# Optimization experiments

Hardware: AMD Instinct MI355X
Metric: run time of the kernel (lower is better)

The kernel has to match this reference:

```python
import jax, jax.numpy as jnp
import numpy as np

DIM = 1024
DIM_HEAD = 128
HEADS = 8
DIM_INNER = DIM_HEAD * HEADS


def setup_inputs() -> dict:
    key = jax.random.key(0)
    k_x, k_qkv, k_out = jax.random.split(key, 3)
    x = jax.random.normal(k_x, (2, 2048, DIM), dtype=jnp.float32)
    gamma = jnp.ones((DIM,), dtype=jnp.float32)
    # nn.Linear weights stored as [out, in]; init ~ U(-1/sqrt(in), 1/sqrt(in))
    w_qkv = jax.random.uniform(k_qkv, (DIM_INNER * 3, DIM), dtype=jnp.float32,
                               minval=-1.0, maxval=1.0) / np.sqrt(DIM)
    w_out = jax.random.uniform(k_out, (DIM, DIM_INNER), dtype=jnp.float32,
                               minval=-1.0, maxval=1.0) / np.sqrt(DIM_INNER)
    return {"x": x, "gamma": gamma, "w_qkv": w_qkv, "w_out": w_out}


def reference(x, gamma, w_qkv, w_out):
    scale_norm = DIM ** 0.5
    scale_attn = DIM_HEAD ** -0.5
    # RMSNorm as written: F.normalize (L2) * sqrt(dim) * gamma
    l2 = jnp.sqrt(jnp.sum(x * x, axis=-1, keepdims=True))
    xn = x / jnp.maximum(l2, 1e-12) * scale_norm * gamma
    # QKV projection: [b, n, 3*h*d]
    qkv = jnp.einsum('bnc,fc->bnf', xn, w_qkv)
    b, n, _ = qkv.shape
    qkv = qkv.reshape(b, n, 3, HEADS, DIM_HEAD)
    q, k, v = (qkv[:, :, 0], qkv[:, :, 1], qkv[:, :, 2])  # [b, n, h, d]
    q = q * scale_attn
    sim = jnp.einsum('bihd,bjhd->bhij', q, k)
    causal_mask = jnp.triu(jnp.ones((n, n), dtype=bool), k=1)
    neg = -jnp.finfo(sim.dtype).max
    sim = jnp.where(causal_mask, neg, sim)
    attn = jax.nn.softmax(sim, axis=-1)
    out = jnp.einsum('bhij,bjhd->bihd', attn, v)
    out = out.reshape(b, n, DIM_INNER)  # merge heads: b n (h d)
    return jnp.einsum('bnf,cf->bnc', out, w_out)
```

## Files before the change

### kernel.cpp

```cpp
#include <hip/hip_runtime.h>

#define SEQ 2048
#define NTOK 4096
#define DIM 1024
#define FQKV 3072
#define SC_ATTN 0.08838834764831843f
#define SC_Q (0.08838834764831843f * 1.4426950408889634f)
#define SC_NORM 32.0f

typedef short short8 __attribute__((ext_vector_type(8)));
typedef float f32x4 __attribute__((ext_vector_type(4)));
typedef unsigned short u16x4 __attribute__((ext_vector_type(4)));

__device__ __forceinline__ unsigned short f2bf(float f) {
    unsigned int u = __float_as_uint(f);
    u += 0x7fffu + ((u >> 16) & 1u);
    return (unsigned short)(u >> 16);
}
__device__ __forceinline__ void gl_lds16(const void* g, void* l) {
    __builtin_amdgcn_global_load_lds((const __attribute__((address_space(1))) void*)g,
                                     (__attribute__((address_space(3))) void*)l, 16, 0, 0);
}

__global__ __launch_bounds__(256) void l2norm_bf16(const float* __restrict__ x,
                                                   const float* __restrict__ gamma,
                                                   unsigned short* __restrict__ xn) {
    int token = blockIdx.x;
    float4 v = ((const float4*)(x + (size_t)token * DIM))[threadIdx.x];
    float ss = v.x * v.x + v.y * v.y + v.z * v.z + v.w * v.w;
#pragma unroll
    for (int off = 32; off > 0; off >>= 1) ss += __shfl_down(ss, off);
    __shared__ float wsum[4];
    if ((threadIdx.x & 63) == 0) wsum[threadIdx.x >> 6] = ss;
    __syncthreads();
    float tot = wsum[0] + wsum[1] + wsum[2] + wsum[3];
    float sc = SC_NORM / fmaxf(sqrtf(tot), 1e-12f);
    float4 g = ((const float4*)gamma)[threadIdx.x];
    u16x4 o;
    o.x = f2bf(v.x * sc * g.x);
    o.y = f2bf(v.y * sc * g.y);
    o.z = f2bf(v.z * sc * g.z);
    o.w = f2bf(v.w * sc * g.w);
    ((u16x4*)(xn + (size_t)token * DIM))[threadIdx.x] = o;
}

__global__ __launch_bounds__(256) void wconv2(const float* __restrict__ wa, unsigned short* __restrict__ oa, int na4,
                                              const float* __restrict__ wb, unsigned short* __restrict__ ob, int nb4) {
    int i = blockIdx.x * 256 + threadIdx.x;
    const float* w; unsigned short* o; int idx;
    if (i < na4) { w = wa; o = oa; idx = i; }
    else { idx = i - na4; if (idx >= nb4) return; w = wb; o = ob; }
    float4 v = ((const float4*)w)[idx];
    u16x4 r;
    r.x = f2bf(v.x); r.y = f2bf(v.y); r.z = f2bf(v.z); r.w = f2bf(v.w);
    ((u16x4*)o)[idx] = r;
}

template<int C_MODE, int TM>
__global__ __launch_bounds__(256) void gemm_bf16(const unsigned short* __restrict__ A,
                                                 const unsigned short* __restrict__ B,
                                                 void* __restrict__ Cv,
                                                 int M, int N, int K) {
    constexpr int MF = TM / 32;
    __shared__ unsigned short As[TM * 64];
    __shared__ unsigned short Bs[128 * 64];

    int lin = blockIdx.y * gridDim.x + blockIdx.x;
    int nwg = gridDim.x * gridDim.y;
    int w = (lin & 7) * (nwg >> 3) + (lin >> 3);
    int bx = w % gridDim.x, by = w / gridDim.x;

    const int bn = bx * 128, bm = by * TM;
    const int tid = threadIdx.x, lane = tid & 63, wv = tid >> 6;
    const int wr = wv >> 1, wc = wv & 1;
    const int l15 = lane & 15, g = lane >> 4;

    f32x4 acc[MF][4] = {};

    auto stage = [&](int k0) {
#pragma unroll
        for (int ia = 0; ia < TM / 32; ++ia) {
            int ci = ia * 256 + wv * 64 + lane;
            int row = ci >> 3, cc = ci & 7;
            int co = (cc ^ (row & 7)) << 3;
            gl_lds16(A + (size_t)(bm + row) * K + k0 + co, &As[(ia * 256 + wv * 64) * 8]);
        }
#pragma unroll
        for (int ib = 0; ib < 4; ++ib) {
            int ci = ib * 256 + wv * 64 + lane;
            int row = ci >> 3, cc = ci & 7;
            int co = (cc ^ (row & 7)) << 3;
            gl_lds16(B + (size_t)(bn + row) * K + k0 + co, &Bs[(ib * 256 + wv * 64) * 8]);
        }
    };

    stage(0);
    asm volatile("s_waitcnt vmcnt(0)\ns_barrier" ::: "memory");

    for (int k0 = 0; k0 < K; k0 += 64) {
        short8 af[2][MF], bf[2][4];
#pragma unroll
        for (int ks = 0; ks < 2; ++ks) {
#pragma unroll
            for (int f = 0; f < MF; ++f) {
                int ra = wr * (TM / 2) + f * 16 + l15;
                af[ks][f] = *(const short8*)&As[ra * 64 + (((ks * 4 + g) ^ (ra & 7)) << 3)];
            }
#pragma unroll
            for (int f = 0; f < 4; ++f) {
                int rb = wc * 64 + f * 16 + l15;
                bf[ks][f] = *(const short8*)&Bs[rb * 64 + (((ks * 4 + g) ^ (rb & 7)) << 3)];
            }
        }
        asm volatile("s_waitcnt lgkmcnt(0)\ns_barrier" ::: "memory");
        if (k0 + 64 < K) stage(k0 + 64);
#pragma unroll
        for (int ks = 0; ks < 2; ++ks)
#pragma unroll
            for (int i = 0; i < MF; ++i)
#pragma unroll
                for (int j = 0; j < 4; ++j)
                    acc[i][j] = __builtin_amdgcn_mfma_f32_16x16x32_bf16(af[ks][i], bf[ks][j], acc[i][j], 0, 0, 0);
        asm volatile("s_waitcnt vmcnt(0)\ns_barrier" ::: "memory");
    }

    if (C_MODE == 0) {
        float* C = (float*)Cv;
#pragma unroll
        for (int i = 0; i < MF; ++i)
#pragma unroll
            for (int j = 0; j < 4; ++j)
#pragma unroll
                for (int v = 0; v < 4; ++v) {
                    int row = bm + wr * (TM / 2) + i * 16 + g * 4 + v;
                    int col = bn + wc * 64 + j * 16 + l15;
                    C[(size_t)row * N + col] = acc[i][j][v];
                }
    } else {
        unsigned short* C = (unsigned short*)Cv;
        float s = (bn < 1024) ? SC_Q : 1.0f;
#pragma unroll
        for (int i = 0; i < MF; ++i)
#pragma unroll
            for (int j = 0; j < 4; ++j)
#pragma unroll
                for (int v = 0; v < 4; ++v) {
                    int row = bm + wr * (TM / 2) + i * 16 + g * 4 + v;
                    int col = bn + wc * 64 + j * 16 + l15;
                    C[(size_t)row * N + col] = f2bf(acc[i][j][v] * s);
                }
    }
}

__global__ __launch_bounds__(256) void transpose_v(const unsigned short* __restrict__ qkv,
                                                   unsigned short* __restrict__ vt) {
    __shared__ unsigned short T[64][72];
    const int t0 = blockIdx.x * 64, d0 = blockIdx.y * 64, bh = blockIdx.z;
    const int b = bh >> 3, h = bh & 7;
    const int tid = threadIdx.x;
#pragma unroll
    for (int p = 0; p < 2; ++p) {
        int r = p * 32 + (tid >> 3), c = tid & 7;
        *(short8*)&T[r][c * 8] =
            *(const short8*)(qkv + (size_t)(b * SEQ + t0 + r) * FQKV + 2048 + h * 128 + d0 + c * 8);
    }
    __syncthreads();
#pragma unroll
    for (int p = 0; p < 2; ++p) {
        int d = p * 32 + (tid >> 3), c = tid & 7;
        short8 v;
#pragma unroll
        for (int j = 0; j < 8; ++j) v[j] = (short)T[c * 8 + j][d];
        *(short8*)(vt + (size_t)(bh * 128 + d0 + d) * SEQ + t0 + c * 8) = v;
    }
}

__global__ __launch_bounds__(256) void attn_mfma(const unsigned short* __restrict__ qkv,
                                                 const unsigned short* __restrict__ vt,
                                                 unsigned short* __restrict__ ao,
                                                 float* __restrict__ po,
                                                 float* __restrict__ pml) {
    __shared__ unsigned short Ks[64 * 128];
    __shared__ unsigned short Vs[128 * 64];
    __shared__ unsigned short Ps[4][16 * 64];
    const int h = blockIdx.y, b = blockIdx.z;
    const int x = blockIdx.x;
    int qblk, jb0, jb1, split, slot;
    if (x < 32) {
        qblk = 31 - (x >> 1);
        int s = x & 1;
        int T = qblk + 1, half = (T + 1) >> 1;
        jb0 = s ? half : 0;
        jb1 = s ? T : half;
        split = 1;
        slot = ((b * 8 + h) * 16 + (qblk - 16)) * 2 + s;
    } else {
        qblk = 47 - x;
        jb0 = 0; jb1 = qblk + 1;
        split = 0; slot = 0;
    }
    const int tid = threadIdx.x, lane = tid & 63, wv = tid >> 6;
    const int l15 = lane & 15, g = lane >> 4;
    const int q0 = qblk * 64;
    const int qrow = q0 + wv * 16 + l15;

    auto stageK = [&](int jb) {
#pragma unroll
        for (int inst = 0; inst < 4; ++inst) {
            int ci = inst * 256 + wv * 64 + lane;
            int rowk = ci >> 4, ck = ci & 15;
            gl_lds16(qkv + (size_t)(b * SEQ + jb * 64 + rowk) * FQKV + 1024 + h * 128
                         + ((ck ^ (rowk & 7)) << 3),
                     &Ks[(inst * 256 + wv * 64) * 8]);
        }
    };
    auto stageV = [&](int jb) {
#pragma unroll
        for (int inst = 0; inst < 4; ++inst) {
            int ci = inst * 256 + wv * 64 + lane;
            int rowv = ci >> 3, cv = ci & 7;
            gl_lds16(vt + (size_t)((b * 8 + h) * 128 + rowv) * SEQ + jb * 64
                        + ((cv ^ (rowv & 7)) << 3),
                     &Vs[(inst * 256 + wv * 64) * 8]);
        }
    };

    short8 qf[4];
    {
        const unsigned short* qb = qkv + (size_t)(b * SEQ + qrow) * FQKV + h * 128;
#pragma unroll
        for (int ks = 0; ks < 4; ++ks) qf[ks] = *(const short8*)(qb + ks * 32 + g * 8);
    }

    float m_r = -1e30f, l_r = 0.f;
    f32x4 o[8] = {};

    stageK(jb0);
    __syncthreads();

    for (int jb = jb0; jb < jb1; ++jb) {
        stageV(jb);

        f32x4 s[4] = {};
        __builtin_amdgcn_s_setprio(1);
#pragma unroll
        for (int ks = 0; ks < 4; ++ks) {
#pragma unroll
            for (int fi = 0; fi < 4; ++fi) {
                int rk = fi * 16 + l15;
                short8 kf = *(const short8*)&Ks[rk * 128 + (((ks * 4 + g) ^ (rk & 7)) << 3)];
                s[fi] = __builtin_amdgcn_mfma_f32_16x16x32_bf16(kf, qf[ks], s[fi], 0, 0, 0);
            }
        }
        __builtin_amdgcn_s_setprio(0);

        if (jb == qblk) {
#pragma unroll
            for (int fi = 0; fi < 4; ++fi)
#pragma unroll
                for (int v = 0; v < 4; ++v) {
                    int kv = q0 + fi * 16 + g * 4 + v;
                    if (kv > qrow) s[fi][v] = -1e30f;
                }
        }

        float mx = -1e30f;
#pragma unroll
        for (int fi = 0; fi < 4; ++fi)
            mx = fmaxf(mx, fmaxf(fmaxf(s[fi][0], s[fi][1]), fmaxf(s[fi][2], s[fi][3])));
        mx = fmaxf(mx, __shfl_xor(mx, 16));
        mx = fmaxf(mx, __shfl_xor(mx, 32));
        if (__any(mx - m_r > 16.0f)) {
            float Mn = fmaxf(m_r, mx);
            float alpha = exp2f(m_r - Mn);
            l_r *= alpha;
            float av[4];
#pragma unroll
            for (int v = 0; v < 4; ++v) av[v] = __shfl(alpha, g * 4 + v);
#pragma unroll
            for (int fn = 0; fn < 8; ++fn) {
                o[fn][0] *= av[0]; o[fn][1] *= av[1]; o[fn][2] *= av[2]; o[fn][3] *= av[3];
            }
            m_r = Mn;
        }

        float ps = 0.f;
#pragma unroll
        for (int fi = 0; fi < 4; ++fi) {
#pragma unroll
            for (int p2 = 0; p2 < 2; ++p2) {
                float e0 = exp2f(s[fi][2 * p2] - m_r);
                float e1 = exp2f(s[fi][2 * p2 + 1] - m_r);
                ps += e0 + e1;
                unsigned short b0 = f2bf(e0), b1 = f2bf(e1);
                int kv = fi * 16 + g * 4 + 2 * p2;
                int addr = l15 * 64 + (((kv >> 3) ^ (l15 & 7)) << 3) + (kv & 7);
                *(unsigned int*)&Ps[wv][addr] = (unsigned int)b0 | ((unsigned int)b1 << 16);
            }
        }
        ps += __shfl_xor(ps, 16);
        ps += __shfl_xor(ps, 32);
        l_r += ps;

        __syncthreads();
        if (jb + 1 < jb1) stageK(jb + 1);

        __builtin_amdgcn_s_setprio(1);
#pragma unroll
        for (int ks = 0; ks < 2; ++ks) {
            short8 pa = *(const short8*)&Ps[wv][l15 * 64 + (((ks * 4 + g) ^ (l15 & 7)) << 3)];
#pragma unroll
            for (int fn = 0; fn < 8; ++fn) {
                int rv = fn * 16 + l15;
                short8 vf = *(const short8*)&Vs[rv * 64 + (((ks * 4 + g) ^ (rv & 7)) << 3)];
                o[fn] = __builtin_amdgcn_mfma_f32_16x16x32_bf16(pa, vf, o[fn], 0, 0, 0);
            }
        }
        __builtin_amdgcn_s_setprio(0);

        __syncthreads();
    }

    if (split) {
        float* od = po + (size_t)slot * (64 * 128);
#pragma unroll
        for (int fn = 0; fn < 8; ++fn)
#pragma unroll
            for (int v = 0; v < 4; ++v)
                od[(wv * 16 + g * 4 + v) * 128 + fn * 16 + l15] = o[fn][v];
        if (g == 0) {
            pml[(size_t)slot * 128 + wv * 16 + l15] = m_r;
            pml[(size_t)slot * 128 + 64 + wv * 16 + l15] = l_r;
        }
    } else {
        float lv[4];
#pragma unroll
        for (int v = 0; v < 4; ++v) lv[v] = 1.0f / __shfl(l_r, g * 4 + v);
#pragma unroll
        for (int fn = 0; fn < 8; ++fn)
#pragma unroll
            for (int v = 0; v < 4; ++v) {
                int row = b * SEQ + q0 + wv * 16 + g * 4 + v;
                ao[(size_t)row * DIM + h * 128 + fn * 16 + l15] = f2bf(o[fn][v] * lv[v]);
            }
    }
}

__global__ __launch_bounds__(256) void attn_combine(const float* __restrict__ po,
                                                    const float* __restrict__ pml,
                                                    unsigned short* __restrict__ ao) {
    int t = blockIdx.x;
    int qi = t & 15, h = (t >> 4) & 7, b = t >> 7;
    int qblk = 16 + qi;
    int slot0 = ((b * 8 + h) * 16 + qi) * 2;
    int row = threadIdx.x >> 2;
    int dp = threadIdx.x & 3;
    float m0 = pml[(size_t)slot0 * 128 + row];
    float l0 = pml[(size_t)slot0 * 128 + 64 + row];
    float m1 = pml[(size_t)(slot0 + 1) * 128 + row];
    float l1 = pml[(size_t)(slot0 + 1) * 128 + 64 + row];
    float M = fmaxf(m0, m1);
    float w0 = exp2f(m0 - M), w1 = exp2f(m1 - M);
    float inv = 1.0f / (w0 * l0 + w1 * l1);
    w0 *= inv; w1 *= inv;
    const float4* O0 = (const float4*)(po + (size_t)slot0 * 8192 + row * 128 + dp * 32);
    const float4* O1 = (const float4*)(po + (size_t)(slot0 + 1) * 8192 + row * 128 + dp * 32);
    unsigned short* dst = ao + ((size_t)(b * SEQ + qblk * 64 + row)) * DIM + h * 128 + dp * 32;
#pragma unroll
    for (int j = 0; j < 8; ++j) {
        float4 a = O0[j], c = O1[j];
        u16x4 r;
        r.x = f2bf(w0 * a.x + w1 * c.x);
        r.y = f2bf(w0 * a.y + w1 * c.y);
        r.z = f2bf(w0 * a.z + w1 * c.z);
        r.w = f2bf(w0 * a.w + w1 * c.w);
        *(u16x4*)(dst + j * 4) = r;
    }
}

extern "C" void kernel_launch(void* const* d_in, const int* in_sizes, int n_in,
                              void* d_out, int out_size, void* d_ws, size_t ws_size,
                              hipStream_t stream) {
    const float* x     = (const float*)d_in[0];
    const float* gamma = (const float*)d_in[1];
    const float* w_qkv = (const float*)d_in[2];
    const float* w_out = (const float*)d_in[3];

    char* ws = (char*)d_ws;
    unsigned short* qkvb = (unsigned short*)ws;
    unsigned short* vtb  = (unsigned short*)(ws + 25165824);
    unsigned short* xnb  = (unsigned short*)(ws + 33554432);
    unsigned short* wqb  = (unsigned short*)(ws + 41943040);
    unsigned short* wob  = (unsigned short*)(ws + 48234496);
    unsigned short* aob  = (unsigned short*)(ws + 50331648);
    float*          pml  = (float*)(ws + 58720256);
    float*          po   = (float*)d_out;

    wconv2<<<4096, 256, 0, stream>>>(w_qkv, wqb, 786432, w_out, wob, 262144);
    l2norm_bf16<<<4096, 256, 0, stream>>>(x, gamma, xnb);
    gemm_bf16<1, 128><<<dim3(24, 32), 256, 0, stream>>>(xnb, wqb, qkvb, NTOK, FQKV, DIM);
    transpose_v<<<dim3(32, 2, 16), 256, 0, stream>>>(qkvb, vtb);
    attn_mfma<<<dim3(48, 8, 2), 256, 0, stream>>>(qkvb, vtb, aob, po, pml);
    attn_combine<<<256, 256, 0, stream>>>(po, pml, aob);
    gemm_bf16<0, 64><<<dim3(8, 64), 256, 0, stream>>>(aob, wob, (float*)d_out, NTOK, DIM, DIM);
}
```

Measured before the change: 119.9 us.

## Rebalance causal attention with variable-width KV splits and bf16 partials

Attention work is now split more finely: query blocks 28-31 get 4 KV splits, blocks 18-27 get 3, blocks 9-17 get 2, and the rest run unsplit, with 73 blocks per head instead of 48. The goal is to even out the triangular causal workload across CUs and cut tail time. Partial outputs are stored as bf16 instead of fp32 to halve scratch traffic. The combine kernel is generalised to merge 2-4 partials. The weight conversion and the L2 norm now run in one prep launch. Costs are more combine work and extra rounding of the partials to bf16.

```diff
diff --git a/kernel.cpp b/kernel.cpp
--- a/kernel.cpp
+++ b/kernel.cpp
@@ -4,7 +4,6 @@
 #define NTOK 4096
 #define DIM 1024
 #define FQKV 3072
-#define SC_ATTN 0.08838834764831843f
 #define SC_Q (0.08838834764831843f * 1.4426950408889634f)
 #define SC_NORM 32.0f
 
@@ -17,43 +16,49 @@
     u += 0x7fffu + ((u >> 16) & 1u);
     return (unsigned short)(u >> 16);
 }
+__device__ __forceinline__ float bf2f(unsigned short b) {
+    return __uint_as_float(((unsigned int)b) << 16);
+}
 __device__ __forceinline__ void gl_lds16(const void* g, void* l) {
     __builtin_amdgcn_global_load_lds((const __attribute__((address_space(1))) void*)g,
                                      (__attribute__((address_space(3))) void*)l, 16, 0, 0);
 }
 
-__global__ __launch_bounds__(256) void l2norm_bf16(const float* __restrict__ x,
-                                                   const float* __restrict__ gamma,
-                                                   unsigned short* __restrict__ xn) {
-    int token = blockIdx.x;
-    float4 v = ((const float4*)(x + (size_t)token * DIM))[threadIdx.x];
-    float ss = v.x * v.x + v.y * v.y + v.z * v.z + v.w * v.w;
-#pragma unroll
-    for (int off = 32; off > 0; off >>= 1) ss += __shfl_down(ss, off);
-    __shared__ float wsum[4];
-    if ((threadIdx.x & 63) == 0) wsum[threadIdx.x >> 6] = ss;
-    __syncthreads();
-    float tot = wsum[0] + wsum[1] + wsum[2] + wsum[3];
-    float sc = SC_NORM / fmaxf(sqrtf(tot), 1e-12f);
-    float4 g = ((const float4*)gamma)[threadIdx.x];
-    u16x4 o;
-    o.x = f2bf(v.x * sc * g.x);
-    o.y = f2bf(v.y * sc * g.y);
-    o.z = f2bf(v.z * sc * g.z);
-    o.w = f2bf(v.w * sc * g.w);
-    ((u16x4*)(xn + (size_t)token * DIM))[threadIdx.x] = o;
-}
-
-__global__ __launch_bounds__(256) void wconv2(const float* __restrict__ wa, unsigned short* __restrict__ oa, int na4,
-                                              const float* __restrict__ wb, unsigned short* __restrict__ ob, int nb4) {
-    int i = blockIdx.x * 256 + threadIdx.x;
-    const float* w; unsigned short* o; int idx;
-    if (i < na4) { w = wa; o = oa; idx = i; }
-    else { idx = i - na4; if (idx >= nb4) return; w = wb; o = ob; }
-    float4 v = ((const float4*)w)[idx];
-    u16x4 r;
-    r.x = f2bf(v.x); r.y = f2bf(v.y); r.z = f2bf(v.z); r.w = f2bf(v.w);
-    ((u16x4*)o)[idx] = r;
+__global__ __launch_bounds__(256) void prep(const float* __restrict__ x,
+                                            const float* __restrict__ gamma,
+                                            unsigned short* __restrict__ xn,
+                                            const float* __restrict__ wq,
+                                            unsigned short* __restrict__ wqb,
+                                            const float* __restrict__ wo,
+                                            unsigned short* __restrict__ wob) {
+    if (blockIdx.x < 4096) {
+        int token = blockIdx.x;
+        float4 v = ((const float4*)(x + (size_t)token * DIM))[threadIdx.x];
+        float ss = v.x * v.x + v.y * v.y + v.z * v.z + v.w * v.w;
+#pragma unroll
+        for (int off = 32; off > 0; off >>= 1) ss += __shfl_down(ss, off);
+        __shared__ float wsum[4];
+        if ((threadIdx.x & 63) == 0) wsum[threadIdx.x >> 6] = ss;
+        __syncthreads();
+        float tot = wsum[0] + wsum[1] + wsum[2] + wsum[3];
+        float sc = SC_NORM / fmaxf(sqrtf(tot), 1e-12f);
+        float4 g = ((const float4*)gamma)[threadIdx.x];
+        u16x4 o;
+        o.x = f2bf(v.x * sc * g.x);
+        o.y = f2bf(v.y * sc * g.y);
+        o.z = f2bf(v.z * sc * g.z);
+        o.w = f2bf(v.w * sc * g.w);
+        ((u16x4*)(xn + (size_t)token * DIM))[threadIdx.x] = o;
+    } else {
+        int i = (blockIdx.x - 4096) * 256 + threadIdx.x;
+        const float* w; unsigned short* o; int idx;
+        if (i < 786432) { w = wq; o = wqb; idx = i; }
+        else            { w = wo; o = wob; idx = i - 786432; }
+        float4 v = ((const float4*)w)[idx];
+        u16x4 r;
+        r.x = f2bf(v.x); r.y = f2bf(v.y); r.z = f2bf(v.z); r.w = f2bf(v.w);
+        ((u16x4*)o)[idx] = r;
+    }
 }
 
 template<int C_MODE, int TM>
@@ -178,27 +183,23 @@
 __global__ __launch_bounds__(256) void attn_mfma(const unsigned short* __restrict__ qkv,
                                                  const unsigned short* __restrict__ vt,
                                                  unsigned short* __restrict__ ao,
-                                                 float* __restrict__ po,
+                                                 unsigned short* __restrict__ po,
                                                  float* __restrict__ pml) {
     __shared__ unsigned short Ks[64 * 128];
     __shared__ unsigned short Vs[128 * 64];
     __shared__ unsigned short Ps[4][16 * 64];
     const int h = blockIdx.y, b = blockIdx.z;
     const int x = blockIdx.x;
-    int qblk, jb0, jb1, split, slot;
-    if (x < 32) {
-        qblk = 31 - (x >> 1);
-        int s = x & 1;
-        int T = qblk + 1, half = (T + 1) >> 1;
-        jb0 = s ? half : 0;
-        jb1 = s ? T : half;
-        split = 1;
-        slot = ((b * 8 + h) * 16 + (qblk - 16)) * 2 + s;
-    } else {
-        qblk = 47 - x;
-        jb0 = 0; jb1 = qblk + 1;
-        split = 0; slot = 0;
-    }
+    int qblk, s, nsp;
+    if (x < 30)      { qblk = 27 - x / 3;               s = x % 3;  nsp = 3; }
+    else if (x < 46) { int i = x - 30; qblk = 31 - (i >> 2); s = i & 3; nsp = 4; }
+    else if (x < 64) { int i = x - 46; qblk = 17 - (i >> 1); s = i & 1; nsp = 2; }
+    else             { qblk = 72 - x;                   s = 0;      nsp = 1; }
+    const int T = qblk + 1;
+    const int jb0 = (s * T) / nsp, jb1 = ((s + 1) * T) / nsp;
+    const int split = (nsp > 1);
+    const int slot = ((b * 8 + h) << 6) + x;
+
     const int tid = threadIdx.x, lane = tid & 63, wv = tid >> 6;
     const int l15 = lane & 15, g = lane >> 4;
     const int q0 = qblk * 64;
@@ -241,7 +242,7 @@
     for (int jb = jb0; jb < jb1; ++jb) {
         stageV(jb);
 
-        f32x4 s[4] = {};
+        f32x4 sv[4] = {};
         __builtin_amdgcn_s_setprio(1);
 #pragma unroll
         for (int ks = 0; ks < 4; ++ks) {
@@ -249,7 +250,7 @@
             for (int fi = 0; fi < 4; ++fi) {
                 int rk = fi * 16 + l15;
                 short8 kf = *(const short8*)&Ks[rk * 128 + (((ks * 4 + g) ^ (rk & 7)) << 3)];
-                s[fi] = __builtin_amdgcn_mfma_f32_16x16x32_bf16(kf, qf[ks], s[fi], 0, 0, 0);
+                sv[fi] = __builtin_amdgcn_mfma_f32_16x16x32_bf16(kf, qf[ks], sv[fi], 0, 0, 0);
             }
         }
         __builtin_amdgcn_s_setprio(0);
@@ -260,14 +261,14 @@
 #pragma unroll
                 for (int v = 0; v < 4; ++v) {
                     int kv = q0 + fi * 16 + g * 4 + v;
-                    if (kv > qrow) s[fi][v] = -1e30f;
+                    if (kv > qrow) sv[fi][v] = -1e30f;
                 }
         }
 
         float mx = -1e30f;
 #pragma unroll
         for (int fi = 0; fi < 4; ++fi)
-            mx = fmaxf(mx, fmaxf(fmaxf(s[fi][0], s[fi][1]), fmaxf(s[fi][2], s[fi][3])));
+            mx = fmaxf(mx, fmaxf(fmaxf(sv[fi][0], sv[fi][1]), fmaxf(sv[fi][2], sv[fi][3])));
         mx = fmaxf(mx, __shfl_xor(mx, 16));
         mx = fmaxf(mx, __shfl_xor(mx, 32));
         if (__any(mx - m_r > 16.0f)) {
@@ -289,8 +290,8 @@
         for (int fi = 0; fi < 4; ++fi) {
 #pragma unroll
             for (int p2 = 0; p2 < 2; ++p2) {
-                float e0 = exp2f(s[fi][2 * p2] - m_r);
-                float e1 = exp2f(s[fi][2 * p2 + 1] - m_r);
+                float e0 = exp2f(sv[fi][2 * p2] - m_r);
+                float e1 = exp2f(sv[fi][2 * p2 + 1] - m_r);
                 ps += e0 + e1;
                 unsigned short b0 = f2bf(e0), b1 = f2bf(e1);
                 int kv = fi * 16 + g * 4 + 2 * p2;
@@ -322,12 +323,12 @@
     }
 
     if (split) {
-        float* od = po + (size_t)slot * (64 * 128);
+        unsigned short* od = po + (size_t)slot * 8192;
 #pragma unroll
         for (int fn = 0; fn < 8; ++fn)
 #pragma unroll
             for (int v = 0; v < 4; ++v)
-                od[(wv * 16 + g * 4 + v) * 128 + fn * 16 + l15] = o[fn][v];
+                od[(wv * 16 + g * 4 + v) * 128 + fn * 16 + l15] = f2bf(o[fn][v]);
         if (g == 0) {
             pml[(size_t)slot * 128 + wv * 16 + l15] = m_r;
             pml[(size_t)slot * 128 + 64 + wv * 16 + l15] = l_r;
@@ -346,35 +347,50 @@
     }
 }
 
-__global__ __launch_bounds__(256) void attn_combine(const float* __restrict__ po,
+__global__ __launch_bounds__(256) void attn_combine(const unsigned short* __restrict__ po,
                                                     const float* __restrict__ pml,
                                                     unsigned short* __restrict__ ao) {
-    int t = blockIdx.x;
-    int qi = t & 15, h = (t >> 4) & 7, b = t >> 7;
-    int qblk = 16 + qi;
-    int slot0 = ((b * 8 + h) * 16 + qi) * 2;
-    int row = threadIdx.x >> 2;
-    int dp = threadIdx.x & 3;
-    float m0 = pml[(size_t)slot0 * 128 + row];
-    float l0 = pml[(size_t)slot0 * 128 + 64 + row];
-    float m1 = pml[(size_t)(slot0 + 1) * 128 + row];
-    float l1 = pml[(size_t)(slot0 + 1) * 128 + 64 + row];
-    float M = fmaxf(m0, m1);
-    float w0 = exp2f(m0 - M), w1 = exp2f(m1 - M);
-    float inv = 1.0f / (w0 * l0 + w1 * l1);
-    w0 *= inv; w1 *= inv;
-    const float4* O0 = (const float4*)(po + (size_t)slot0 * 8192 + row * 128 + dp * 32);
-    const float4* O1 = (const float4*)(po + (size_t)(slot0 + 1) * 8192 + row * 128 + dp * 32);
+    const int qblk = 9 + blockIdx.x, h = blockIdx.y, b = blockIdx.z;
+    int base, n;
+    if (qblk >= 28)      { base = 30 + (31 - qblk) * 4; n = 4; }
+    else if (qblk >= 18) { base = (27 - qblk) * 3;      n = 3; }
+    else                 { base = 46 + (17 - qblk) * 2; n = 2; }
+    const int slot0 = ((b * 8 + h) << 6) + base;
+    const int row = threadIdx.x >> 2, dp = threadIdx.x & 3;
+
+    float M = -1e30f;
+#pragma unroll
+    for (int s2 = 0; s2 < 4; ++s2)
+        if (s2 < n) M = fmaxf(M, pml[(size_t)(slot0 + s2) * 128 + row]);
+    float denom = 0.f;
+#pragma unroll
+    for (int s2 = 0; s2 < 4; ++s2)
+        if (s2 < n) denom += exp2f(pml[(size_t)(slot0 + s2) * 128 + row] - M)
+                             * pml[(size_t)(slot0 + s2) * 128 + 64 + row];
+    float inv = 1.0f / denom;
+
+    float acc[32] = {};
+#pragma unroll
+    for (int s2 = 0; s2 < 4; ++s2)
+        if (s2 < n) {
+            float wgt = exp2f(pml[(size_t)(slot0 + s2) * 128 + row] - M) * inv;
+            const unsigned short* ob = po + (size_t)(slot0 + s2) * 8192 + row * 128 + dp * 32;
+#pragma unroll
+            for (int j = 0; j < 4; ++j) {
+                short8 pv = *(const short8*)(ob + j * 8);
+#pragma unroll
+                for (int e = 0; e < 8; ++e)
+                    acc[j * 8 + e] += wgt * bf2f((unsigned short)pv[e]);
+            }
+        }
+
     unsigned short* dst = ao + ((size_t)(b * SEQ + qblk * 64 + row)) * DIM + h * 128 + dp * 32;
 #pragma unroll
-    for (int j = 0; j < 8; ++j) {
-        float4 a = O0[j], c = O1[j];
-        u16x4 r;
-        r.x = f2bf(w0 * a.x + w1 * c.x);
-        r.y = f2bf(w0 * a.y + w1 * c.y);
-        r.z = f2bf(w0 * a.z + w1 * c.z);
-        r.w = f2bf(w0 * a.w + w1 * c.w);
-        *(u16x4*)(dst + j * 4) = r;
+    for (int j = 0; j < 4; ++j) {
+        short8 r;
+#pragma unroll
+        for (int e = 0; e < 8; ++e) r[e] = (short)f2bf(acc[j * 8 + e]);
+        *(short8*)(dst + j * 8) = r;
     }
 }
 
@@ -393,14 +409,13 @@
     unsigned short* wqb  = (unsigned short*)(ws + 41943040);
     unsigned short* wob  = (unsigned short*)(ws + 48234496);
     unsigned short* aob  = (unsigned short*)(ws + 50331648);
-    float*          pml  = (float*)(ws + 58720256);
-    float*          po   = (float*)d_out;
-
-    wconv2<<<4096, 256, 0, stream>>>(w_qkv, wqb, 786432, w_out, wob, 262144);
-    l2norm_bf16<<<4096, 256, 0, stream>>>(x, gamma, xnb);
+    float*          pml  = (float*)(ws + 41943040);
+    unsigned short* po   = (unsigned short*)d_out;
+
+    prep<<<8192, 256, 0, stream>>>(x, gamma, xnb, w_qkv, wqb, w_out, wob);
     gemm_bf16<1, 128><<<dim3(24, 32), 256, 0, stream>>>(xnb, wqb, qkvb, NTOK, FQKV, DIM);
     transpose_v<<<dim3(32, 2, 16), 256, 0, stream>>>(qkvb, vtb);
-    attn_mfma<<<dim3(48, 8, 2), 256, 0, stream>>>(qkvb, vtb, aob, po, pml);
-    attn_combine<<<256, 256, 0, stream>>>(po, pml, aob);
+    attn_mfma<<<dim3(73, 8, 2), 256, 0, stream>>>(qkvb, vtb, aob, po, pml);
+    attn_combine<<<dim3(23, 8, 2), 256, 0, stream>>>(po, pml, aob);
     gemm_bf16<0, 64><<<dim3(8, 64), 256, 0, stream>>>(aob, wob, (float*)d_out, NTOK, DIM, DIM);
 }
```

After: 118.2 us. Within noise of the previous version (-1.4%).
